# Performance work log

Measured on AMD Instinct MI355X. Metric: run time of the kernel, lower is better.

## Reference

```python
import jax, jax.numpy as jnp
import numpy as np

N_NODES = 50000
N_EDGES = 1600000
NUM_REL = 4
IN_F = 256
OUT_F = 128


def setup_inputs() -> dict:
    key = jax.random.key(0)
    k1, k2, k3 = jax.random.split(key, 3)
    X = jax.random.normal(k1, (N_NODES, IN_F), dtype=jnp.float32)
    # Glorot-ish scale for the per-relation GraphConv weights
    W = jax.random.normal(k2, (NUM_REL, IN_F, OUT_F), dtype=jnp.float32) * (1.0 / np.sqrt(IN_F))
    edge_index = jax.random.randint(k3, (NUM_REL, 2, N_EDGES), 0, N_NODES, dtype=jnp.int64 if jax.config.jax_enable_x64 else jnp.int32)
    return {"X": X, "W": W, "edge_index": edge_index}


def _graph_conv(X, Wr, src, dst, n_nodes):
    """DGL GraphConv, norm='both', bias=False, allow_zero_in_degree=True."""
    ones = jnp.ones(src.shape, dtype=X.dtype)
    out_deg = jax.ops.segment_sum(ones, src, num_segments=n_nodes)
    in_deg = jax.ops.segment_sum(ones, dst, num_segments=n_nodes)
    out_norm = jnp.clip(out_deg, 1.0, None) ** -0.5  # [N]
    in_norm = jnp.clip(in_deg, 1.0, None) ** -0.5    # [N]
    # in_feats > out_feats: apply weight first (same math, cheaper messages)
    h = (X * out_norm[:, None]) @ Wr                 # [N, out]
    agg = jax.ops.segment_sum(h[src], dst, num_segments=n_nodes)  # [N, out]
    return agg * in_norm[:, None]


def reference(X, W, edge_index):
    n_nodes = X.shape[0]
    num_rel = W.shape[0]
    Z = jnp.zeros((n_nodes, W.shape[2]), dtype=X.dtype)
    for r in range(num_rel):  # small fixed loop over relations
        Z = Z + _graph_conv(X, W[r], edge_index[r, 0], edge_index[r, 1], n_nodes)
    return Z
```

## Files before the change

kernel.cpp:

```cpp
#include <hip/hip_runtime.h>

#define IN_F 256
#define OUT_F 128
#define NUM_REL 4
#define BN 64
#define PBX 64
#define PT 512
#define WPB 8

typedef unsigned int u32;
typedef unsigned short u16;
typedef unsigned char u8;

typedef __attribute__((ext_vector_type(8))) short bf16x8;
typedef __attribute__((ext_vector_type(4))) float f32x4;

static __device__ __forceinline__ u16 f32_to_bf16(float f) {
    union { float f; u32 u; } c; c.f = f;
    u32 u = c.u;
    u32 r = (u + 0x7fffu + ((u >> 16) & 1u)) >> 16;
    return (u16)r;
}
static __device__ __forceinline__ float bf16lo(u32 v) {
    union { u32 u; float f; } c; c.u = v << 16; return c.f;
}
static __device__ __forceinline__ float bf16hi(u32 v) {
    union { u32 u; float f; } c; c.u = v & 0xffff0000u; return c.f;
}

__global__ __launch_bounds__(PT) void p1_hist(const int* __restrict__ EI, u32* __restrict__ ghd,
                                              u32* __restrict__ ghs, int E, int NB, int r0, int CH) {
    int rr = blockIdx.y, x = blockIdx.x;
    int r = r0 + rr;
    const int* src = EI + (size_t)(2 * r) * E;
    const int* dst = src + E;
    extern __shared__ u32 sh[];
    u32* hd = sh;
    u32* hs = sh + WPB * NB;
    int t = threadIdx.x, w = t >> 6, lane = t & 63;
    for (int i = t; i < 2 * WPB * NB; i += PT) sh[i] = 0;
    __syncthreads();
    u32* hdw = hd + w * NB;
    u32* hsw = hs + w * NB;
    int CHW = CH / WPB;
    int lo = x * CH + w * CHW;
    int hi = min(E, lo + CHW);
    if ((E & 3) == 0) {
        for (int e = lo + lane * 4; e < hi; e += 64 * 4) {
            int4 s4 = *(const int4*)(src + e);
            int4 d4 = *(const int4*)(dst + e);
            atomicAdd(&hdw[d4.x >> 6], 1u); atomicAdd(&hsw[s4.x >> 6], 1u);
            atomicAdd(&hdw[d4.y >> 6], 1u); atomicAdd(&hsw[s4.y >> 6], 1u);
            atomicAdd(&hdw[d4.z >> 6], 1u); atomicAdd(&hsw[s4.z >> 6], 1u);
            atomicAdd(&hdw[d4.w >> 6], 1u); atomicAdd(&hsw[s4.w >> 6], 1u);
        }
    } else {
        for (int e = lo + lane; e < hi; e += 64) {
            atomicAdd(&hdw[dst[e] >> 6], 1u);
            atomicAdd(&hsw[src[e] >> 6], 1u);
        }
    }
    __syncthreads();
    for (int i = t; i < NB * WPB; i += PT) {
        int b = i >> 3, w2 = i & 7;
        size_t bin = (size_t)(rr * NB + b);
        ghd[bin * (PBX * WPB) + x * WPB + w2] = hd[w2 * NB + b];
        ghs[bin * (PBX * WPB) + x * WPB + w2] = hs[w2 * NB + b];
    }
}

__global__ __launch_bounds__(512) void p2a_scan(u32* __restrict__ ghd, u32* __restrict__ ghs,
                                                u32* __restrict__ bintot, int BINS) {
    int wid = blockIdx.x;
    u32* g = (wid < BINS) ? ghd : ghs;
    int bin = (wid < BINS) ? wid : wid - BINS;
    int t = threadIdx.x, lane = t & 63, w = t >> 6;
    __shared__ u32 wpart[WPB];
    u32 c = g[(size_t)bin * (PBX * WPB) + t];
    u32 x = c;
    #pragma unroll
    for (int s = 1; s < 64; s <<= 1) {
        u32 y = __shfl_up(x, s);
        if (lane >= s) x += y;
    }
    if (lane == 63) wpart[w] = x;
    __syncthreads();
    if (w == 0 && lane < WPB) {
        u32 wx = wpart[lane];
        #pragma unroll
        for (int s = 1; s < WPB; s <<= 1) {
            u32 wy = __shfl_up(wx, s);
            if (lane >= s) wx += wy;
        }
        wpart[lane] = wx;
    }
    __syncthreads();
    u32 woff = (w > 0) ? wpart[w - 1] : 0;
    g[(size_t)bin * (PBX * WPB) + t] = x + woff - c;
    if (t == 511) bintot[wid] = x + woff;
}

__global__ __launch_bounds__(1024) void p2b_scan(const u32* __restrict__ bintot,
                                                 u32* __restrict__ binbase_d,
                                                 u32* __restrict__ binbase_s, int BINS) {
    __shared__ u32 wsum[16];
    __shared__ u32 carry;
    int t = threadIdx.x;
    int lane = t & 63, wv = t >> 6;
    for (int seg = 0; seg < 2; seg++) {
        const u32* in = bintot + (size_t)seg * BINS;
        u32* out = seg ? binbase_s : binbase_d;
        if (t == 0) carry = 0;
        __syncthreads();
        for (int base = 0; base < BINS; base += 1024) {
            int i = base + t;
            u32 v = (i < BINS) ? in[i] : 0;
            u32 x = v;
            #pragma unroll
            for (int s = 1; s < 64; s <<= 1) {
                u32 y = __shfl_up(x, s);
                if (lane >= s) x += y;
            }
            if (lane == 63) wsum[wv] = x;
            __syncthreads();
            if (wv == 0 && lane < 16) {
                u32 wx = wsum[lane];
                #pragma unroll
                for (int s = 1; s < 16; s <<= 1) {
                    u32 wy = __shfl_up(wx, s);
                    if (lane >= s) wx += wy;
                }
                wsum[lane] = wx;
            }
            __syncthreads();
            u32 woff = (wv > 0) ? wsum[wv - 1] : 0;
            u32 incl = x + woff;
            u32 c0 = carry;
            if (i < BINS) out[i] = c0 + incl - v;
            __syncthreads();
            if (t == 1023) carry = c0 + incl;
            __syncthreads();
        }
        if (t == 0) out[BINS] = carry;
        __syncthreads();
    }
}

__global__ __launch_bounds__(PT) void p3_scatter(const int* __restrict__ EI,
                                                 const u32* __restrict__ ghd, const u32* __restrict__ ghs,
                                                 const u32* __restrict__ binbase_d, const u32* __restrict__ binbase_s,
                                                 u32* __restrict__ part_dst, u8* __restrict__ part_src,
                                                 int E, int NB, int r0, int CH) {
    int rr = blockIdx.y, x = blockIdx.x;
    int r = r0 + rr;
    const int* src = EI + (size_t)(2 * r) * E;
    const int* dst = src + E;
    extern __shared__ u32 sh[];
    u32* cd = sh;
    u32* cs = sh + WPB * NB;
    int t = threadIdx.x, w = t >> 6, lane = t & 63;
    for (int i = t; i < NB * WPB; i += PT) {
        int b = i >> 3, w2 = i & 7;
        size_t bin = (size_t)(rr * NB + b);
        cd[w2 * NB + b] = binbase_d[bin] + ghd[bin * (PBX * WPB) + x * WPB + w2];
        cs[w2 * NB + b] = binbase_s[bin] + ghs[bin * (PBX * WPB) + x * WPB + w2];
    }
    __syncthreads();
    u32* cdw = cd + w * NB;
    u32* csw = cs + w * NB;
    int CHW = CH / WPB;
    int lo = x * CH + w * CHW;
    int hi = min(E, lo + CHW);
    if ((E & 3) == 0) {
        for (int e = lo + lane * 4; e < hi; e += 64 * 4) {
            int4 s4 = *(const int4*)(src + e);
            int4 d4 = *(const int4*)(dst + e);
            #pragma unroll
            for (int k = 0; k < 4; k++) {
                int sv = (&s4.x)[k], dv = (&d4.x)[k];
                int db = dv >> 6, sb = sv >> 6;
                u32 pos = atomicAdd(&cdw[db], 1u);
                part_dst[pos] = ((u32)sv << 6) | (u32)(dv & 63);
                u32 pos2 = atomicAdd(&csw[sb], 1u);
                part_src[pos2] = (u8)(sv & 63);
            }
        }
    } else {
        for (int e = lo + lane; e < hi; e += 64) {
            int sv = src[e], dv = dst[e];
            int db = dv >> 6, sb = sv >> 6;
            u32 pos = atomicAdd(&cdw[db], 1u);
            part_dst[pos] = ((u32)sv << 6) | (u32)(dv & 63);
            u32 pos2 = atomicAdd(&csw[sb], 1u);
            part_src[pos2] = (u8)(sv & 63);
        }
    }
}

__global__ __launch_bounds__(256) void p4_sort(const u32* __restrict__ part_dst,
                                               const u32* __restrict__ binbase_d,
                                               const u8* __restrict__ part_src,
                                               const u32* __restrict__ binbase_s,
                                               u32* __restrict__ offs, u16* __restrict__ sorted,
                                               float* __restrict__ out_norm,
                                               int N, int NB, int nrel) {
    int b = blockIdx.x, rr = blockIdx.y;
    int bin = rr * NB + b;
    __shared__ u32 cnt[BN];
    int t = threadIdx.x;
    if (t < BN) cnt[t] = 0;
    __syncthreads();
    {
        u32 slo = binbase_s[bin], shi = binbase_s[bin + 1];
        for (u32 i = slo + t; i < shi; i += 256) atomicAdd(&cnt[part_src[i]], 1u);
    }
    __syncthreads();
    if (t < BN) {
        int node = b * BN + t;
        if (node < N) out_norm[(size_t)rr * N + node] = rsqrtf((float)max(cnt[t], 1u));
        cnt[t] = 0;
    }
    __syncthreads();
    u32 lo = binbase_d[bin], hi = binbase_d[bin + 1];
    for (u32 i = lo + t; i < hi; i += 256) atomicAdd(&cnt[part_dst[i] & 63u], 1u);
    __syncthreads();
    if (t < BN) {
        u32 c = cnt[t];
        u32 x = c;
        #pragma unroll
        for (int s = 1; s < 64; s <<= 1) {
            u32 y = __shfl_up(x, s);
            if (t >= s) x += y;
        }
        u32 excl = x - c;
        int node = b * BN + t;
        if (node < N) offs[(size_t)rr * N + node] = lo + excl;
        cnt[t] = excl;
    }
    __syncthreads();
    for (u32 i = lo + t; i < hi; i += 256) {
        u32 p = part_dst[i];
        u32 pos = atomicAdd(&cnt[p & 63u], 1u);
        sorted[lo + pos] = (u16)(p >> 6);
    }
    if (b == 0 && rr == 0 && t == 0)
        offs[(size_t)nrel * N] = binbase_d[(size_t)nrel * NB];
}

__global__ void prep_kernel(const float* __restrict__ X, const float* __restrict__ W,
                            u16* __restrict__ Xb, u16* __restrict__ BImg,
                            int N, int nxb, int nwt) {
    int idx = blockIdx.x * 256 + threadIdx.x;
    if (idx < nxb) {
        int ci = idx & 1023;
        int S = (idx >> 10) & 3;
        int R = idx >> 12;
        int mg = ci >> 7, kgl = (ci >> 4) & 7, rw = ci & 15;
        int row = R * 128 + mg * 16 + rw;
        int k0 = S * 64 + kgl * 8;
        u16 o[8] = {0, 0, 0, 0, 0, 0, 0, 0};
        if (row < N) {
            const float* xp = X + (size_t)row * IN_F + k0;
            float4 v0 = *(const float4*)xp;
            float4 v1 = *(const float4*)(xp + 4);
            o[0] = f32_to_bf16(v0.x); o[1] = f32_to_bf16(v0.y);
            o[2] = f32_to_bf16(v0.z); o[3] = f32_to_bf16(v0.w);
            o[4] = f32_to_bf16(v1.x); o[5] = f32_to_bf16(v1.y);
            o[6] = f32_to_bf16(v1.z); o[7] = f32_to_bf16(v1.w);
        }
        *(uint4*)(Xb + (size_t)idx * 8) = *(const uint4*)o;
    } else if (idx < nxb + nwt) {
        int wi = idx - nxb;
        int r = wi >> 12, q = wi & 4095;
        int ng = q >> 9, kg = (q >> 4) & 31, c = q & 15;
        const float* Wr = W + (size_t)r * IN_F * OUT_F;
        u16 o[8];
        #pragma unroll
        for (int j = 0; j < 8; j++)
            o[j] = f32_to_bf16(Wr[(size_t)(8 * kg + j) * OUT_F + 16 * ng + c]);
        *(uint4*)(BImg + (size_t)wi * 8) = *(const uint4*)o;
    }
}

__global__ __launch_bounds__(256) void gemm_kernel(const u16* __restrict__ Xb,
                                                   const u16* __restrict__ BImg,
                                                   const float* __restrict__ out_norm,
                                                   u16* __restrict__ h, int N, int r0) {
    int rr = blockIdx.y;
    int r = r0 + rr;
    int R = blockIdx.x;
    int row0 = R * 128;
    __shared__ short Alds[8192];
    __shared__ short Blds[32768];
    int t = threadIdx.x;
    int lane = t & 63, w = t >> 6;
    int wm = w >> 1, wn = w & 1;

    const uint4* bsrc = (const uint4*)(BImg + (size_t)r * 32768);
    uint4* bdst = (uint4*)Blds;
    #pragma unroll
    for (int i = 0; i < 16; i++) bdst[i * 256 + t] = bsrc[i * 256 + t];

    f32x4 acc[4][4];
    #pragma unroll
    for (int mi = 0; mi < 4; mi++)
        #pragma unroll
        for (int ni = 0; ni < 4; ni++) acc[mi][ni] = (f32x4){0.f, 0.f, 0.f, 0.f};

    const uint4* xb4 = (const uint4*)Xb + (size_t)R * 4096;
    uint4 areg[4];
    #pragma unroll
    for (int i = 0; i < 4; i++) areg[i] = xb4[i * 256 + t];

    for (int S = 0; S < 4; S++) {
        uint4* adst = (uint4*)Alds;
        #pragma unroll
        for (int i = 0; i < 4; i++) adst[i * 256 + t] = areg[i];
        __syncthreads();
        if (S < 3) {
            #pragma unroll
            for (int i = 0; i < 4; i++) areg[i] = xb4[(size_t)(S + 1) * 1024 + i * 256 + t];
        }
        #pragma unroll
        for (int kf = 0; kf < 2; kf++) {
            bf16x8 a[4], b[4];
            #pragma unroll
            for (int mi = 0; mi < 4; mi++)
                a[mi] = *(const bf16x8*)(Alds + (wm * 4 + mi) * 1024 + kf * 512 + lane * 8);
            #pragma unroll
            for (int ni = 0; ni < 4; ni++)
                b[ni] = *(const bf16x8*)(Blds + (wn * 4 + ni) * 4096 + S * 1024 + kf * 512 + lane * 8);
            #pragma unroll
            for (int mi = 0; mi < 4; mi++)
                #pragma unroll
                for (int ni = 0; ni < 4; ni++)
                    acc[mi][ni] = __builtin_amdgcn_mfma_f32_16x16x32_bf16(a[mi], b[ni], acc[mi][ni], 0, 0, 0);
        }
        __syncthreads();
    }

    const float* nrm = out_norm + (size_t)rr * N;
    u16* hr = h + (size_t)rr * N * OUT_F;
    #pragma unroll
    for (int mi = 0; mi < 4; mi++) {
        #pragma unroll
        for (int rg = 0; rg < 4; rg++) {
            int row = row0 + wm * 64 + mi * 16 + (lane >> 4) * 4 + rg;
            if (row >= N) continue;
            float nv = nrm[row];
            #pragma unroll
            for (int ni = 0; ni < 4; ni++) {
                int col = wn * 64 + ni * 16 + (lane & 15);
                hr[(size_t)row * OUT_F + col] = f32_to_bf16(acc[mi][ni][rg] * nv);
            }
        }
    }
}

__global__ __launch_bounds__(256) void aggregate_kernel(const u16* __restrict__ sorted,
                                                        const u32* __restrict__ offs,
                                                        const u16* __restrict__ h,
                                                        float* __restrict__ Z,
                                                        int N, int nrel, int accflag) {
    int wid = (blockIdx.x * 256 + threadIdx.x) >> 6;
    int lane = threadIdx.x & 63;
    int g = lane >> 4, l16 = lane & 15;
    int dst = wid * 4 + g;
    int dstc = (dst < N) ? dst : (N - 1);
    float t[8] = {0.f, 0.f, 0.f, 0.f, 0.f, 0.f, 0.f, 0.f};
    for (int rr = 0; rr < nrel; rr++) {
        u32 b = offs[(size_t)rr * N + dstc];
        u32 e = offs[(size_t)rr * N + dstc + 1];
        u32 cnt = (dst < N) ? (e - b) : 0u;
        const uint4* hr = (const uint4*)(h + (size_t)rr * N * OUT_F);
        float a[8] = {0.f, 0.f, 0.f, 0.f, 0.f, 0.f, 0.f, 0.f};
        u32 j = 0;
        for (; j + 8 <= cnt; j += 8) {
            u32 ids[8];
            #pragma unroll
            for (int q = 0; q < 8; q++) ids[q] = (u32)sorted[b + j + q];
            uint4 rv[8];
            #pragma unroll
            for (int q = 0; q < 8; q++) rv[q] = hr[(size_t)ids[q] * 16 + l16];
            #pragma unroll
            for (int q = 0; q < 8; q++) {
                a[0] += bf16lo(rv[q].x); a[1] += bf16hi(rv[q].x);
                a[2] += bf16lo(rv[q].y); a[3] += bf16hi(rv[q].y);
                a[4] += bf16lo(rv[q].z); a[5] += bf16hi(rv[q].z);
                a[6] += bf16lo(rv[q].w); a[7] += bf16hi(rv[q].w);
            }
        }
        for (; j < cnt; j++) {
            uint4 rv = hr[(size_t)sorted[b + j] * 16 + l16];
            a[0] += bf16lo(rv.x); a[1] += bf16hi(rv.x);
            a[2] += bf16lo(rv.y); a[3] += bf16hi(rv.y);
            a[4] += bf16lo(rv.z); a[5] += bf16hi(rv.z);
            a[6] += bf16lo(rv.w); a[7] += bf16hi(rv.w);
        }
        float inr = rsqrtf((float)max(cnt, 1u));
        #pragma unroll
        for (int k = 0; k < 8; k++) t[k] += inr * a[k];
    }
    if (dst < N) {
        float4* zp = (float4*)(Z + (size_t)dst * OUT_F + l16 * 8);
        if (accflag) {
            float4 z0 = zp[0], z1 = zp[1];
            z0.x += t[0]; z0.y += t[1]; z0.z += t[2]; z0.w += t[3];
            z1.x += t[4]; z1.y += t[5]; z1.z += t[6]; z1.w += t[7];
            zp[0] = z0; zp[1] = z1;
        } else {
            zp[0] = make_float4(t[0], t[1], t[2], t[3]);
            zp[1] = make_float4(t[4], t[5], t[6], t[7]);
        }
    }
}

extern "C" void kernel_launch(void* const* d_in, const int* in_sizes, int n_in,
                              void* d_out, int out_size, void* d_ws, size_t ws_size,
                              hipStream_t stream) {
    const float* X = (const float*)d_in[0];
    const float* W = (const float*)d_in[1];
    const int* EI = (const int*)d_in[2];
    float* Z = (float*)d_out;
    const int N = in_sizes[0] / IN_F;
    const int E = in_sizes[2] / (NUM_REL * 2);
    const int NB = (N + BN - 1) / BN;
    const int RBcnt = (N + 127) / 128;
    const int CH = (((E + PBX - 1) / PBX) + 31) & ~31;
    const size_t privLds = (size_t)2 * WPB * NB * 4;

    size_t sorted_o, offs_o, out_norm_o, bbd_o, bbs_o, xb_o, bimg_o, h_o,
           ghd_o, ghs_o, bintot_o, part_dst_o, part_src_o;
    auto layout = [&](int nb) -> size_t {
        size_t cur = 0;
        auto alloc = [&](size_t bytes) {
            size_t o = cur; cur = (cur + bytes + 255) & ~(size_t)255; return o;
        };
        int BINS = nb * NB;
        size_t TE = (size_t)nb * E;
        sorted_o   = alloc(TE * 2);
        offs_o     = alloc(((size_t)nb * N + 1) * 4);
        out_norm_o = alloc((size_t)nb * N * 4);
        bbd_o      = alloc((size_t)(BINS + 1) * 4);
        bbs_o      = alloc((size_t)(BINS + 1) * 4);
        xb_o       = alloc((size_t)RBcnt * 4096 * 16);
        bimg_o     = alloc((size_t)NUM_REL * 4096 * 16);
        h_o        = alloc((size_t)nb * N * OUT_F * 2);
        size_t hend = cur;
        size_t ov = h_o;
        auto oalloc = [&](size_t bytes) {
            size_t o = ov; ov = (ov + bytes + 255) & ~(size_t)255; return o;
        };
        ghd_o      = oalloc((size_t)BINS * PBX * WPB * 4);
        ghs_o      = oalloc((size_t)BINS * PBX * WPB * 4);
        bintot_o   = oalloc((size_t)2 * BINS * 4);
        part_dst_o = oalloc(TE * 4);
        part_src_o = oalloc(TE);
        return (ov > hend) ? ov : hend;
    };
    int nb = NUM_REL;
    while (nb > 1 && layout(nb) > ws_size) nb >>= 1;
    layout(nb);
    char* ws = (char*)d_ws;
    const int nbatches = (NUM_REL + nb - 1) / nb;

    u16* xb = (u16*)(ws + xb_o);
    u16* bimg = (u16*)(ws + bimg_o);

    int nxb = RBcnt * 4096;
    int nwt = NUM_REL * 4096;
    prep_kernel<<<(nxb + nwt + 255) / 256, 256, 0, stream>>>(X, W, xb, bimg, N, nxb, nwt);

    if (nbatches > 1)
        hipMemsetAsync(d_out, 0, (size_t)N * OUT_F * sizeof(float), stream);

    for (int r0 = 0; r0 < NUM_REL; r0 += nb) {
        int cur = min(nb, NUM_REL - r0);
        int BINS = cur * NB;
        u16* sorted   = (u16*)(ws + sorted_o);
        u32* offs     = (u32*)(ws + offs_o);
        float* out_norm = (float*)(ws + out_norm_o);
        u32* bbd      = (u32*)(ws + bbd_o);
        u32* bbs      = (u32*)(ws + bbs_o);
        u16* h        = (u16*)(ws + h_o);
        u32* ghd      = (u32*)(ws + ghd_o);
        u32* ghs      = (u32*)(ws + ghs_o);
        u32* bintot   = (u32*)(ws + bintot_o);
        u32* part_dst = (u32*)(ws + part_dst_o);
        u8* part_src  = (u8*)(ws + part_src_o);

        p1_hist<<<dim3(PBX, cur), PT, privLds, stream>>>(EI, ghd, ghs, E, NB, r0, CH);
        p2a_scan<<<2 * BINS, 512, 0, stream>>>(ghd, ghs, bintot, BINS);
        p2b_scan<<<1, 1024, 0, stream>>>(bintot, bbd, bbs, BINS);
        p3_scatter<<<dim3(PBX, cur), PT, privLds, stream>>>(
            EI, ghd, ghs, bbd, bbs, part_dst, part_src, E, NB, r0, CH);
        p4_sort<<<dim3(NB, cur), 256, 0, stream>>>(
            part_dst, bbd, part_src, bbs, offs, sorted, out_norm, N, NB, cur);
        gemm_kernel<<<dim3(RBcnt, cur), 256, 0, stream>>>(xb, bimg, out_norm, h, N, r0);
        aggregate_kernel<<<(N + 15) / 16, 256, 0, stream>>>(
            sorted, offs, h, Z, N, cur, (nbatches > 1) ? 1 : 0);
    }
}
```

Before: 461.9 us.

## Widen counting-sort buckets from 64 to 512 nodes per bin

Raises the per-bin node range of the two-level counting sort from 64 to 512 nodes. This cuts the bin count by eight, which shrinks the per-block histograms, the global histogram arrays and the scan work in p1/p2/p3. p4_sort now runs 512 threads per block and does a two-level block-wide scan over 512 local counters. The cost is 16-bit instead of 8-bit part_src entries, more LDS atomic contention inside each p4 block, and fewer p4 blocks to spread across the GPU.

```diff
diff --git a/kernel.cpp b/kernel.cpp
--- a/kernel.cpp
+++ b/kernel.cpp
@@ -3,7 +3,7 @@
 #define IN_F 256
 #define OUT_F 128
 #define NUM_REL 4
-#define BN 64
+#define BK2 512
 #define PBX 64
 #define PT 512
 #define WPB 8
@@ -29,19 +29,19 @@
 }
 
 __global__ __launch_bounds__(PT) void p1_hist(const int* __restrict__ EI, u32* __restrict__ ghd,
-                                              u32* __restrict__ ghs, int E, int NB, int r0, int CH) {
+                                              u32* __restrict__ ghs, int E, int NB2, int r0, int CH) {
     int rr = blockIdx.y, x = blockIdx.x;
     int r = r0 + rr;
     const int* src = EI + (size_t)(2 * r) * E;
     const int* dst = src + E;
     extern __shared__ u32 sh[];
     u32* hd = sh;
-    u32* hs = sh + WPB * NB;
+    u32* hs = sh + WPB * NB2;
     int t = threadIdx.x, w = t >> 6, lane = t & 63;
-    for (int i = t; i < 2 * WPB * NB; i += PT) sh[i] = 0;
-    __syncthreads();
-    u32* hdw = hd + w * NB;
-    u32* hsw = hs + w * NB;
+    for (int i = t; i < 2 * WPB * NB2; i += PT) sh[i] = 0;
+    __syncthreads();
+    u32* hdw = hd + w * NB2;
+    u32* hsw = hs + w * NB2;
     int CHW = CH / WPB;
     int lo = x * CH + w * CHW;
     int hi = min(E, lo + CHW);
@@ -49,23 +49,23 @@
         for (int e = lo + lane * 4; e < hi; e += 64 * 4) {
             int4 s4 = *(const int4*)(src + e);
             int4 d4 = *(const int4*)(dst + e);
-            atomicAdd(&hdw[d4.x >> 6], 1u); atomicAdd(&hsw[s4.x >> 6], 1u);
-            atomicAdd(&hdw[d4.y >> 6], 1u); atomicAdd(&hsw[s4.y >> 6], 1u);
-            atomicAdd(&hdw[d4.z >> 6], 1u); atomicAdd(&hsw[s4.z >> 6], 1u);
-            atomicAdd(&hdw[d4.w >> 6], 1u); atomicAdd(&hsw[s4.w >> 6], 1u);
+            atomicAdd(&hdw[d4.x >> 9], 1u); atomicAdd(&hsw[s4.x >> 9], 1u);
+            atomicAdd(&hdw[d4.y >> 9], 1u); atomicAdd(&hsw[s4.y >> 9], 1u);
+            atomicAdd(&hdw[d4.z >> 9], 1u); atomicAdd(&hsw[s4.z >> 9], 1u);
+            atomicAdd(&hdw[d4.w >> 9], 1u); atomicAdd(&hsw[s4.w >> 9], 1u);
         }
     } else {
         for (int e = lo + lane; e < hi; e += 64) {
-            atomicAdd(&hdw[dst[e] >> 6], 1u);
-            atomicAdd(&hsw[src[e] >> 6], 1u);
-        }
-    }
-    __syncthreads();
-    for (int i = t; i < NB * WPB; i += PT) {
+            atomicAdd(&hdw[dst[e] >> 9], 1u);
+            atomicAdd(&hsw[src[e] >> 9], 1u);
+        }
+    }
+    __syncthreads();
+    for (int i = t; i < NB2 * WPB; i += PT) {
         int b = i >> 3, w2 = i & 7;
-        size_t bin = (size_t)(rr * NB + b);
-        ghd[bin * (PBX * WPB) + x * WPB + w2] = hd[w2 * NB + b];
-        ghs[bin * (PBX * WPB) + x * WPB + w2] = hs[w2 * NB + b];
+        size_t bin = (size_t)(rr * NB2 + b);
+        ghd[bin * (PBX * WPB) + x * WPB + w2] = hd[w2 * NB2 + b];
+        ghs[bin * (PBX * WPB) + x * WPB + w2] = hs[w2 * NB2 + b];
     }
 }
 
@@ -149,25 +149,25 @@
 __global__ __launch_bounds__(PT) void p3_scatter(const int* __restrict__ EI,
                                                  const u32* __restrict__ ghd, const u32* __restrict__ ghs,
                                                  const u32* __restrict__ binbase_d, const u32* __restrict__ binbase_s,
-                                                 u32* __restrict__ part_dst, u8* __restrict__ part_src,
-                                                 int E, int NB, int r0, int CH) {
+                                                 u32* __restrict__ part_dst, u16* __restrict__ part_src,
+                                                 int E, int NB2, int r0, int CH) {
     int rr = blockIdx.y, x = blockIdx.x;
     int r = r0 + rr;
     const int* src = EI + (size_t)(2 * r) * E;
     const int* dst = src + E;
     extern __shared__ u32 sh[];
     u32* cd = sh;
-    u32* cs = sh + WPB * NB;
+    u32* cs = sh + WPB * NB2;
     int t = threadIdx.x, w = t >> 6, lane = t & 63;
-    for (int i = t; i < NB * WPB; i += PT) {
+    for (int i = t; i < NB2 * WPB; i += PT) {
         int b = i >> 3, w2 = i & 7;
-        size_t bin = (size_t)(rr * NB + b);
-        cd[w2 * NB + b] = binbase_d[bin] + ghd[bin * (PBX * WPB) + x * WPB + w2];
-        cs[w2 * NB + b] = binbase_s[bin] + ghs[bin * (PBX * WPB) + x * WPB + w2];
-    }
-    __syncthreads();
-    u32* cdw = cd + w * NB;
-    u32* csw = cs + w * NB;
+        size_t bin = (size_t)(rr * NB2 + b);
+        cd[w2 * NB2 + b] = binbase_d[bin] + ghd[bin * (PBX * WPB) + x * WPB + w2];
+        cs[w2 * NB2 + b] = binbase_s[bin] + ghs[bin * (PBX * WPB) + x * WPB + w2];
+    }
+    __syncthreads();
+    u32* cdw = cd + w * NB2;
+    u32* csw = cs + w * NB2;
     int CHW = CH / WPB;
     int lo = x * CH + w * CHW;
     int hi = min(E, lo + CHW);
@@ -178,73 +178,81 @@
             #pragma unroll
             for (int k = 0; k < 4; k++) {
                 int sv = (&s4.x)[k], dv = (&d4.x)[k];
-                int db = dv >> 6, sb = sv >> 6;
+                int db = dv >> 9, sb = sv >> 9;
                 u32 pos = atomicAdd(&cdw[db], 1u);
-                part_dst[pos] = ((u32)sv << 6) | (u32)(dv & 63);
+                part_dst[pos] = ((u32)sv << 9) | (u32)(dv & 511);
                 u32 pos2 = atomicAdd(&csw[sb], 1u);
-                part_src[pos2] = (u8)(sv & 63);
+                part_src[pos2] = (u16)(sv & 511);
             }
         }
     } else {
         for (int e = lo + lane; e < hi; e += 64) {
             int sv = src[e], dv = dst[e];
-            int db = dv >> 6, sb = sv >> 6;
+            int db = dv >> 9, sb = sv >> 9;
             u32 pos = atomicAdd(&cdw[db], 1u);
-            part_dst[pos] = ((u32)sv << 6) | (u32)(dv & 63);
+            part_dst[pos] = ((u32)sv << 9) | (u32)(dv & 511);
             u32 pos2 = atomicAdd(&csw[sb], 1u);
-            part_src[pos2] = (u8)(sv & 63);
-        }
-    }
-}
-
-__global__ __launch_bounds__(256) void p4_sort(const u32* __restrict__ part_dst,
+            part_src[pos2] = (u16)(sv & 511);
+        }
+    }
+}
+
+__global__ __launch_bounds__(512) void p4_sort(const u32* __restrict__ part_dst,
                                                const u32* __restrict__ binbase_d,
-                                               const u8* __restrict__ part_src,
+                                               const u16* __restrict__ part_src,
                                                const u32* __restrict__ binbase_s,
                                                u32* __restrict__ offs, u16* __restrict__ sorted,
                                                float* __restrict__ out_norm,
-                                               int N, int NB, int nrel) {
+                                               int N, int NB2, int nrel) {
     int b = blockIdx.x, rr = blockIdx.y;
-    int bin = rr * NB + b;
-    __shared__ u32 cnt[BN];
+    int bin = rr * NB2 + b;
+    __shared__ u32 cntA[BK2];
+    __shared__ u32 cnt[BK2];
+    __shared__ u32 wpart[WPB];
     int t = threadIdx.x;
-    if (t < BN) cnt[t] = 0;
+    int lane = t & 63, w = t >> 6;
+    cntA[t] = 0;
+    cnt[t] = 0;
     __syncthreads();
     {
         u32 slo = binbase_s[bin], shi = binbase_s[bin + 1];
-        for (u32 i = slo + t; i < shi; i += 256) atomicAdd(&cnt[part_src[i]], 1u);
-    }
-    __syncthreads();
-    if (t < BN) {
-        int node = b * BN + t;
-        if (node < N) out_norm[(size_t)rr * N + node] = rsqrtf((float)max(cnt[t], 1u));
-        cnt[t] = 0;
-    }
-    __syncthreads();
+        for (u32 i = slo + t; i < shi; i += 512) atomicAdd(&cntA[part_src[i] & 511u], 1u);
+    }
     u32 lo = binbase_d[bin], hi = binbase_d[bin + 1];
-    for (u32 i = lo + t; i < hi; i += 256) atomicAdd(&cnt[part_dst[i] & 63u], 1u);
-    __syncthreads();
-    if (t < BN) {
-        u32 c = cnt[t];
-        u32 x = c;
-        #pragma unroll
-        for (int s = 1; s < 64; s <<= 1) {
-            u32 y = __shfl_up(x, s);
-            if (t >= s) x += y;
-        }
-        u32 excl = x - c;
-        int node = b * BN + t;
-        if (node < N) offs[(size_t)rr * N + node] = lo + excl;
-        cnt[t] = excl;
-    }
-    __syncthreads();
-    for (u32 i = lo + t; i < hi; i += 256) {
+    for (u32 i = lo + t; i < hi; i += 512) atomicAdd(&cnt[part_dst[i] & 511u], 1u);
+    __syncthreads();
+    int node = b * BK2 + t;
+    if (node < N) out_norm[(size_t)rr * N + node] = rsqrtf((float)max(cntA[t], 1u));
+    u32 c = cnt[t];
+    u32 x = c;
+    #pragma unroll
+    for (int s = 1; s < 64; s <<= 1) {
+        u32 y = __shfl_up(x, s);
+        if (lane >= s) x += y;
+    }
+    if (lane == 63) wpart[w] = x;
+    __syncthreads();
+    if (w == 0 && lane < WPB) {
+        u32 wx = wpart[lane];
+        #pragma unroll
+        for (int s = 1; s < WPB; s <<= 1) {
+            u32 wy = __shfl_up(wx, s);
+            if (lane >= s) wx += wy;
+        }
+        wpart[lane] = wx;
+    }
+    __syncthreads();
+    u32 excl = x - c + ((w > 0) ? wpart[w - 1] : 0);
+    if (node < N) offs[(size_t)rr * N + node] = lo + excl;
+    cnt[t] = excl;
+    __syncthreads();
+    for (u32 i = lo + t; i < hi; i += 512) {
         u32 p = part_dst[i];
-        u32 pos = atomicAdd(&cnt[p & 63u], 1u);
-        sorted[lo + pos] = (u16)(p >> 6);
+        u32 pos = atomicAdd(&cnt[p & 511u], 1u);
+        sorted[lo + pos] = (u16)(p >> 9);
     }
     if (b == 0 && rr == 0 && t == 0)
-        offs[(size_t)nrel * N] = binbase_d[(size_t)nrel * NB];
+        offs[(size_t)nrel * N] = binbase_d[(size_t)nrel * NB2];
 }
 
 __global__ void prep_kernel(const float* __restrict__ X, const float* __restrict__ W,
@@ -424,10 +432,10 @@
     float* Z = (float*)d_out;
     const int N = in_sizes[0] / IN_F;
     const int E = in_sizes[2] / (NUM_REL * 2);
-    const int NB = (N + BN - 1) / BN;
+    const int NB2 = (N + BK2 - 1) / BK2;
     const int RBcnt = (N + 127) / 128;
     const int CH = (((E + PBX - 1) / PBX) + 31) & ~31;
-    const size_t privLds = (size_t)2 * WPB * NB * 4;
+    const size_t privLds = (size_t)2 * WPB * NB2 * 4;
 
     size_t sorted_o, offs_o, out_norm_o, bbd_o, bbs_o, xb_o, bimg_o, h_o,
            ghd_o, ghs_o, bintot_o, part_dst_o, part_src_o;
@@ -436,7 +444,7 @@
         auto alloc = [&](size_t bytes) {
             size_t o = cur; cur = (cur + bytes + 255) & ~(size_t)255; return o;
         };
-        int BINS = nb * NB;
+        int BINS = nb * NB2;
         size_t TE = (size_t)nb * E;
         sorted_o   = alloc(TE * 2);
         offs_o     = alloc(((size_t)nb * N + 1) * 4);
@@ -455,7 +463,7 @@
         ghs_o      = oalloc((size_t)BINS * PBX * WPB * 4);
         bintot_o   = oalloc((size_t)2 * BINS * 4);
         part_dst_o = oalloc(TE * 4);
-        part_src_o = oalloc(TE);
+        part_src_o = oalloc(TE * 2);
         return (ov > hend) ? ov : hend;
     };
     int nb = NUM_REL;
@@ -476,7 +484,7 @@
 
     for (int r0 = 0; r0 < NUM_REL; r0 += nb) {
         int cur = min(nb, NUM_REL - r0);
-        int BINS = cur * NB;
+        int BINS = cur * NB2;
         u16* sorted   = (u16*)(ws + sorted_o);
         u32* offs     = (u32*)(ws + offs_o);
         float* out_norm = (float*)(ws + out_norm_o);
@@ -487,15 +495,15 @@
         u32* ghs      = (u32*)(ws + ghs_o);
         u32* bintot   = (u32*)(ws + bintot_o);
         u32* part_dst = (u32*)(ws + part_dst_o);
-        u8* part_src  = (u8*)(ws + part_src_o);
-
-        p1_hist<<<dim3(PBX, cur), PT, privLds, stream>>>(EI, ghd, ghs, E, NB, r0, CH);
+        u16* part_src = (u16*)(ws + part_src_o);
+
+        p1_hist<<<dim3(PBX, cur), PT, privLds, stream>>>(EI, ghd, ghs, E, NB2, r0, CH);
         p2a_scan<<<2 * BINS, 512, 0, stream>>>(ghd, ghs, bintot, BINS);
         p2b_scan<<<1, 1024, 0, stream>>>(bintot, bbd, bbs, BINS);
         p3_scatter<<<dim3(PBX, cur), PT, privLds, stream>>>(
-            EI, ghd, ghs, bbd, bbs, part_dst, part_src, E, NB, r0, CH);
-        p4_sort<<<dim3(NB, cur), 256, 0, stream>>>(
-            part_dst, bbd, part_src, bbs, offs, sorted, out_norm, N, NB, cur);
+            EI, ghd, ghs, bbd, bbs, part_dst, part_src, E, NB2, r0, CH);
+        p4_sort<<<dim3(NB2, cur), 512, 0, stream>>>(
+            part_dst, bbd, part_src, bbs, offs, sorted, out_norm, N, NB2, cur);
         gemm_kernel<<<dim3(RBcnt, cur), 256, 0, stream>>>(xb, bimg, out_norm, h, N, r0);
         aggregate_kernel<<<(N + 15) / 16, 256, 0, stream>>>(
             sorted, offs, h, Z, N, cur, (nbatches > 1) ? 1 : 0);
```

New measurement: 418.2 us. -9.5%, faster.
